# Kernel tuning notes

Measured on AMD Instinct MI355X. Metric: run time of the kernel, lower is better.

The kernel has to match this reference:

```python
import jax, jax.numpy as jnp
import numpy as np

EPS = 1e-3  # keras LayerNormalization default epsilon


def _ln(x, g, b):
    m = jnp.mean(x, axis=-1, keepdims=True)
    v = jnp.mean(jnp.square(x - m), axis=-1, keepdims=True)
    return (x - m) * jax.lax.rsqrt(v + EPS) * g + b


def setup_inputs() -> dict:
    key = jax.random.key(0)
    B, T, C, H = 64, 256, 1024, 16
    D = C // H
    ks = jax.random.split(key, 16)
    s = 0.02
    return {
        "x": jax.random.normal(ks[0], (B, T, C), jnp.float32),
        # per-head q/k/v projections (no bias), stacked over heads [H, C, D]
        "wq": jax.random.normal(ks[1], (H, C, D), jnp.float32) * s,
        "wk": jax.random.normal(ks[2], (H, C, D), jnp.float32) * s,
        "wv": jax.random.normal(ks[3], (H, C, D), jnp.float32) * s,
        "w_proj": jax.random.normal(ks[4], (C, C), jnp.float32) * s,
        "b_proj": jnp.zeros((C,), jnp.float32),
        # FFN: C -> 4C (relu) -> C
        "w1": jax.random.normal(ks[5], (C, 4 * C), jnp.float32) * s,
        "b1": jnp.zeros((4 * C,), jnp.float32),
        "w2": jax.random.normal(ks[6], (4 * C, C), jnp.float32) * s,
        "b2": jnp.zeros((C,), jnp.float32),
        # LayerNorm params: ln1 (pre-attn), ln2 (pre-ffn), ln3 (inside FeedForward)
        "g1": jnp.ones((C,), jnp.float32), "be1": jnp.zeros((C,), jnp.float32),
        "g2": jnp.ones((C,), jnp.float32), "be2": jnp.zeros((C,), jnp.float32),
        "g3": jnp.ones((C,), jnp.float32), "be3": jnp.zeros((C,), jnp.float32),
    }


def reference(x, wq, wk, wv, w_proj, b_proj, w1, b1, w2, b2,
              g1, be1, g2, be2, g3, be3):
    B, T, C = x.shape
    # --- multi-head causal self-attention on LN1(x) ---
    h = _ln(x, g1, be1)
    q = jnp.einsum('btc,hcd->bhtd', h, wq)
    k = jnp.einsum('btc,hcd->bhtd', h, wk)
    v = jnp.einsum('btc,hcd->bhtd', h, wv)
    # NOTE: original scales by C**-0.5 with C = n_embd (full dim), not head_size
    scores = jnp.einsum('bhtd,bhsd->bhts', q, k) * (C ** -0.5)
    causal = jnp.tril(jnp.ones((T, T), dtype=bool))
    scores = jnp.where(causal, scores, -jnp.inf)
    attn = jax.nn.softmax(scores, axis=-1)  # dropout is identity at inference
    out = jnp.einsum('bhts,bhsd->bhtd', attn, v)
    out = out.transpose(0, 2, 1, 3).reshape(B, T, C)  # concat heads
    out = out @ w_proj + b_proj
    x = x + out
    # --- FeedForward block (contains its own residual + LayerNorm) ---
    y = _ln(x, g2, be2)
    z = jax.nn.relu(y @ w1 + b1) @ w2 + b2
    return x + _ln(y + z, g3, be3)
```

## Files before the change

### kernel.cpp

```cpp
#include <hip/hip_runtime.h>

typedef __bf16 bf16_t;
typedef __bf16 bf16x8 __attribute__((ext_vector_type(8)));
typedef float f32x4 __attribute__((ext_vector_type(4)));

#define LN_EPS 1e-3f

__device__ __forceinline__ void gload_lds16(const void* g, void* l) {
    __builtin_amdgcn_global_load_lds(
        (__attribute__((address_space(1))) void*)(g),
        (__attribute__((address_space(3))) void*)(l), 16, 0, 0);
}

__global__ __launch_bounds__(256)
void transpose_f32_bf16(const float* __restrict__ in, bf16_t* __restrict__ outp,
                        int ldi, int ldo)
{
    __shared__ float tile[64][65];
    const int k0 = blockIdx.x * 64, n0 = blockIdx.y * 64;
    const int tid = threadIdx.x;
    const int r = tid >> 2;
    const int q = tid & 3;
    const float* src = in + (long)(k0 + r) * ldi + n0 + q * 16;
#pragma unroll
    for (int j = 0; j < 4; ++j) {
        float4 v = *(const float4*)(src + j * 4);
        tile[r][q * 16 + j * 4 + 0] = v.x;
        tile[r][q * 16 + j * 4 + 1] = v.y;
        tile[r][q * 16 + j * 4 + 2] = v.z;
        tile[r][q * 16 + j * 4 + 3] = v.w;
    }
    __syncthreads();
    union { bf16_t e[16]; uint4 u[2]; } pk;
#pragma unroll
    for (int j = 0; j < 16; ++j) pk.e[j] = (bf16_t)tile[q * 16 + j][r];
    bf16_t* dst = outp + (long)(n0 + r) * ldo + k0 + q * 16;
    *(uint4*)(dst)     = pk.u[0];
    *(uint4*)(dst + 8) = pk.u[1];
}

__global__ __launch_bounds__(256)
void pack_qkv_t(const float* __restrict__ wq, const float* __restrict__ wk,
                const float* __restrict__ wv, bf16_t* __restrict__ outp)
{
    __shared__ float tile[64][65];
    const int m   = blockIdx.y;
    const int sel = m >> 4, h = m & 15;
    const float* in = ((sel == 0) ? wq : (sel == 1) ? wk : wv) + (long)h * 65536;
    bf16_t* out = outp + ((long)sel * 1024 + h * 64) * 1024;
    const int k0 = blockIdx.x * 64;
    const int tid = threadIdx.x;
    const int r = tid >> 2;
    const int q = tid & 3;
    const float* src = in + (long)(k0 + r) * 64 + q * 16;
#pragma unroll
    for (int j = 0; j < 4; ++j) {
        float4 v = *(const float4*)(src + j * 4);
        tile[r][q * 16 + j * 4 + 0] = v.x;
        tile[r][q * 16 + j * 4 + 1] = v.y;
        tile[r][q * 16 + j * 4 + 2] = v.z;
        tile[r][q * 16 + j * 4 + 3] = v.w;
    }
    __syncthreads();
    union { bf16_t e[16]; uint4 u[2]; } pk;
#pragma unroll
    for (int j = 0; j < 16; ++j) pk.e[j] = (bf16_t)tile[q * 16 + j][r];
    bf16_t* dst = out + (long)r * 1024 + k0 + q * 16;
    *(uint4*)(dst)     = pk.u[0];
    *(uint4*)(dst + 8) = pk.u[1];
}

__global__ __launch_bounds__(256)
void ln_fwd(const float* __restrict__ in, const float* __restrict__ g,
            const float* __restrict__ be, bf16_t* __restrict__ outp)
{
    const long row = blockIdx.x;
    const int t = threadIdx.x;
    float4 v = ((const float4*)(in + row * 1024))[t];
    float s  = v.x + v.y + v.z + v.w;
    float sq = v.x * v.x + v.y * v.y + v.z * v.z + v.w * v.w;
#pragma unroll
    for (int off = 1; off < 64; off <<= 1) {
        s  += __shfl_xor(s, off);
        sq += __shfl_xor(sq, off);
    }
    __shared__ float red[8];
    if ((t & 63) == 0) { red[(t >> 6) * 2] = s; red[(t >> 6) * 2 + 1] = sq; }
    __syncthreads();
    s  = red[0] + red[2] + red[4] + red[6];
    sq = red[1] + red[3] + red[5] + red[7];
    float mean = s * 0.0009765625f;
    float var  = sq * 0.0009765625f - mean * mean;
    float rstd = rsqrtf(var + LN_EPS);
    float4 gv = ((const float4*)g)[t];
    float4 bv = ((const float4*)be)[t];
    union { bf16_t h[4]; uint2 u; } pk;
    pk.h[0] = (bf16_t)((v.x - mean) * rstd * gv.x + bv.x);
    pk.h[1] = (bf16_t)((v.y - mean) * rstd * gv.y + bv.y);
    pk.h[2] = (bf16_t)((v.z - mean) * rstd * gv.z + bv.z);
    pk.h[3] = (bf16_t)((v.w - mean) * rstd * gv.w + bv.w);
    *(uint2*)(outp + row * 1024 + t * 4) = pk.u;
}

__global__ __launch_bounds__(256)
void ln3_kernel(const bf16_t* __restrict__ in, const float* __restrict__ g,
                const float* __restrict__ be, float* outp, const float* res)
{
    const long row = blockIdx.x;
    const int t = threadIdx.x;
    union { uint2 u; bf16_t h[4]; } pk;
    pk.u = *(const uint2*)(in + row * 1024 + t * 4);
    float v0 = (float)pk.h[0], v1 = (float)pk.h[1], v2 = (float)pk.h[2], v3 = (float)pk.h[3];
    float s  = v0 + v1 + v2 + v3;
    float sq = v0 * v0 + v1 * v1 + v2 * v2 + v3 * v3;
#pragma unroll
    for (int off = 1; off < 64; off <<= 1) {
        s  += __shfl_xor(s, off);
        sq += __shfl_xor(sq, off);
    }
    __shared__ float red[8];
    if ((t & 63) == 0) { red[(t >> 6) * 2] = s; red[(t >> 6) * 2 + 1] = sq; }
    __syncthreads();
    s  = red[0] + red[2] + red[4] + red[6];
    sq = red[1] + red[3] + red[5] + red[7];
    float mean = s * 0.0009765625f;
    float var  = sq * 0.0009765625f - mean * mean;
    float rstd = rsqrtf(var + LN_EPS);
    float4 gv = ((const float4*)g)[t];
    float4 bv = ((const float4*)be)[t];
    float4 rv = ((const float4*)(res + row * 1024))[t];
    float4 ov;
    ov.x = rv.x + (v0 - mean) * rstd * gv.x + bv.x;
    ov.y = rv.y + (v1 - mean) * rstd * gv.y + bv.y;
    ov.z = rv.z + (v2 - mean) * rstd * gv.z + bv.z;
    ov.w = rv.w + (v3 - mean) * rstd * gv.w + bv.w;
    ((float4*)outp)[row * 256 + t] = ov;
}

template<int MODE>
__global__ __launch_bounds__(512, 2)
void gemm_bt(const bf16_t* __restrict__ Ap, const bf16_t* __restrict__ Bp,
             void* outp, const float* __restrict__ bias,
             const void* addp, int M, int N, int K)
{
    __shared__ __attribute__((aligned(16))) bf16_t As0[256 * 64];
    __shared__ __attribute__((aligned(16))) bf16_t As1[256 * 64];
    __shared__ __attribute__((aligned(16))) bf16_t As2[256 * 64];
    __shared__ __attribute__((aligned(16))) bf16_t Bs0[256 * 64];
    __shared__ __attribute__((aligned(16))) bf16_t Bs1[256 * 64];

    const int tid  = threadIdx.x;
    const int w    = tid >> 6, lane = tid & 63;
    const int l16  = lane & 15, lg = lane >> 4;
    const int wm   = w >> 2, wn = w & 3;
    const int srow = lane >> 3;
    const int sslot = lane & 7;

    const int gx  = gridDim.x;
    const int gy  = gridDim.y;
    const int nwg = gx * gy;
    const int bid = blockIdx.y * gx + blockIdx.x;
    const int cpx = nwg >> 3;
    const int sid = (bid & 7) * cpx + (bid >> 3);
    const long m0 = (long)(sid / gy) * 256;
    const long n0 = (long)(sid % gy) * 256;
    const int nkt = K >> 6;

    f32x4 acc[8][4] = {};
    bf16x8 a[4][2], b0[2][2], b1[2][2];

    auto STAGEH = [&](const bf16_t* src, long row0, int kt, bf16_t* dst, int h) {
#pragma unroll
        for (int i = 0; i < 2; ++i) {
            int r  = h * 128 + w * 16 + i * 8 + srow;
            int ss = sslot ^ (r & 7);
            gload_lds16(src + (row0 + r) * (long)K + (long)kt * 64 + ss * 8,
                        dst + (h * 128 + w * 16 + i * 8) * 64);
        }
    };

#define LDA_M(buf, mh) do {                                               \
    _Pragma("unroll") for (int j = 0; j < 4; ++j)                         \
    _Pragma("unroll") for (int kk = 0; kk < 2; ++kk) {                    \
        int r  = wm * 128 + (mh) * 64 + j * 16 + l16;                     \
        int ss = (kk * 4 + lg) ^ (r & 7);                                 \
        a[j][kk] = *(const bf16x8*)&buf[r * 64 + ss * 8];                 \
    } } while (0)

#define LDB_M(dst, buf, nh) do {                                          \
    _Pragma("unroll") for (int n = 0; n < 2; ++n)                         \
    _Pragma("unroll") for (int kk = 0; kk < 2; ++kk) {                    \
        int r  = wn * 64 + ((nh) * 2 + n) * 16 + l16;                     \
        int ss = (kk * 4 + lg) ^ (r & 7);                                 \
        dst[n][kk] = *(const bf16x8*)&buf[r * 64 + ss * 8];               \
    } } while (0)

#define MMA_M(bv, mh, nh) do {                                            \
    __builtin_amdgcn_s_setprio(1);                                        \
    _Pragma("unroll") for (int j = 0; j < 4; ++j)                         \
    _Pragma("unroll") for (int n = 0; n < 2; ++n)                         \
    _Pragma("unroll") for (int kk = 0; kk < 2; ++kk)                      \
        acc[(mh) * 4 + j][(nh) * 2 + n] =                                 \
            __builtin_amdgcn_mfma_f32_16x16x32_bf16(                      \
                a[j][kk], bv[n][kk], acc[(mh) * 4 + j][(nh) * 2 + n],     \
                0, 0, 0);                                                 \
    __builtin_amdgcn_s_setprio(0);                                        \
} while (0)

#define PRE_MFMA() do { __builtin_amdgcn_s_barrier();                     \
    asm volatile("s_waitcnt lgkmcnt(0)" ::: "memory");                    \
    __builtin_amdgcn_sched_barrier(0); } while (0)

    STAGEH(Ap, m0, 0, As0, 0); STAGEH(Ap, m0, 0, As0, 1);
    STAGEH(Bp, n0, 0, Bs0, 0); STAGEH(Bp, n0, 0, Bs0, 1);
    STAGEH(Ap, m0, 1, As1, 0); STAGEH(Ap, m0, 1, As1, 1);
    asm volatile("s_waitcnt vmcnt(0)" ::: "memory");
    __builtin_amdgcn_s_barrier();
    __builtin_amdgcn_sched_barrier(0);

    bf16_t *Ar = As0, *An1 = As1, *An2 = As2;
    bf16_t *Br = Bs0, *Bw = Bs1;

    for (int c = 0; c < nkt; ++c) {
        const bool pfa = (c + 2 < nkt);
        const bool pfb = (c + 1 < nkt);

        LDA_M(Ar, 0); LDB_M(b0, Br, 0);
        if (pfb) { STAGEH(Bp, n0, c + 1, Bw, 0); STAGEH(Bp, n0, c + 1, Bw, 1); }
        if (pfa) STAGEH(Ap, m0, c + 2, An2, 0);
        PRE_MFMA(); MMA_M(b0, 0, 0); __builtin_amdgcn_s_barrier();
        LDB_M(b1, Br, 1);
        PRE_MFMA(); MMA_M(b1, 0, 1); __builtin_amdgcn_s_barrier();
        LDA_M(Ar, 1);
        if (pfa) STAGEH(Ap, m0, c + 2, An2, 1);
        PRE_MFMA(); MMA_M(b1, 1, 1); __builtin_amdgcn_s_barrier();
        if (pfa) { asm volatile("s_waitcnt vmcnt(4)" ::: "memory"); }
        else     { asm volatile("s_waitcnt vmcnt(0)" ::: "memory"); }
        __builtin_amdgcn_s_barrier();
        __builtin_amdgcn_sched_barrier(0);
        MMA_M(b0, 1, 0); __builtin_amdgcn_s_barrier();

        bf16_t* t = Ar; Ar = An1; An1 = An2; An2 = t;
        t = Br; Br = Bw; Bw = t;
    }

#pragma unroll
    for (int fm = 0; fm < 8; ++fm) {
#pragma unroll
        for (int fn = 0; fn < 4; ++fn) {
            const long gcol = n0 + wn * 64 + fn * 16 + l16;
            float bv = 0.f;
            if (MODE != 0 && MODE != 4) bv = bias[gcol];
            const long grow0 = m0 + wm * 128 + fm * 16 + lg * 4;
            if (MODE == 4 && gcol >= 2048) {
                union { bf16_t h[4]; uint2 u; } pk;
#pragma unroll
                for (int e = 0; e < 4; ++e) pk.h[e] = (bf16_t)acc[fm][fn][e];
                const int hh = (int)(gcol >> 6) - 32;
                const int d  = (int)gcol & 63;
                const long bb = grow0 >> 8;
                const int s0  = (int)grow0 & 255;
                *(uint2*)((bf16_t*)addp + ((bb * 16 + hh) * 64 + d) * 256 + s0) = pk.u;
                continue;
            }
#pragma unroll
            for (int e = 0; e < 4; ++e) {
                const long grow = grow0 + e;
                float v = acc[fm][fn][e];
                if (MODE == 0 || MODE == 4) {
                    ((bf16_t*)outp)[grow * N + gcol] = (bf16_t)v;
                } else if (MODE == 1) {
                    v += bv + ((const float*)addp)[grow * N + gcol];
                    ((float*)outp)[grow * N + gcol] = v;
                } else if (MODE == 2) {
                    v += bv; v = v > 0.f ? v : 0.f;
                    ((bf16_t*)outp)[grow * N + gcol] = (bf16_t)v;
                } else {
                    v += bv + (float)((const bf16_t*)addp)[grow * N + gcol];
                    ((bf16_t*)outp)[grow * N + gcol] = (bf16_t)v;
                }
            }
        }
    }
#undef LDA_M
#undef LDB_M
#undef MMA_M
#undef PRE_MFMA
}

__global__ __launch_bounds__(256)
void attn_kernel(const bf16_t* __restrict__ qkv, const bf16_t* __restrict__ vt,
                 bf16_t* __restrict__ outp)
{
    __shared__ __attribute__((aligned(16))) bf16_t Kt[2][64 * 64];
    __shared__ __attribute__((aligned(16))) bf16_t Vt[2][64 * 64];
    __shared__ __attribute__((aligned(16))) bf16_t Ps[4][16 * 72];

    const int tid = threadIdx.x, w = tid >> 6, lane = tid & 63;
    const int l16 = lane & 15, lg = lane >> 4;
    const int b = blockIdx.x >> 4, hh = blockIdx.x & 15;
    const bf16_t* pq = qkv + (long)(b * 256) * 3072 + hh * 64;
    const bf16_t* pv = vt + (long)blockIdx.x * 64 * 256;
    const int sr8 = lane >> 3;
    const int sl  = lane & 7;

    bf16x8 qf[4][2];
#pragma unroll
    for (int fm = 0; fm < 4; ++fm)
#pragma unroll
        for (int kk = 0; kk < 2; ++kk)
            qf[fm][kk] = *(const bf16x8*)(pq + (long)(fm * 64 + w * 16 + l16) * 3072
                                          + kk * 32 + lg * 8);

    f32x4 o[4][4] = {};
    float mrun[4][4], lrun[4][4];
#pragma unroll
    for (int i = 0; i < 4; ++i)
#pragma unroll
        for (int j = 0; j < 4; ++j) { mrun[i][j] = -__builtin_inff(); lrun[i][j] = 0.f; }

    auto STAGE = [&](int st, int bb) {
#pragma unroll
        for (int i = 0; i < 2; ++i) {
            int r  = w * 16 + i * 8 + sr8;
            int ss = sl ^ (r & 7);
            gload_lds16(pq + (long)(st * 64 + r) * 3072 + 1024 + ss * 8,
                        &Kt[bb][(w * 16 + i * 8) * 64]);
            gload_lds16(pv + (long)r * 256 + st * 64 + ss * 8,
                        &Vt[bb][(w * 16 + i * 8) * 64]);
        }
    };

    STAGE(0, 0);
    asm volatile("s_waitcnt vmcnt(0)" ::: "memory");
    __syncthreads();

#pragma unroll
    for (int st = 0; st < 4; ++st) {
        const int cb = st & 1;
        if (st < 3) STAGE(st + 1, cb ^ 1);

        f32x4 s[4][4] = {};
#pragma unroll
        for (int ks = 0; ks < 2; ++ks) {
            bf16x8 kb[4];
#pragma unroll
            for (int fs = 0; fs < 4; ++fs)
                kb[fs] = *(const bf16x8*)&Kt[cb][(fs * 16 + l16) * 64
                                               + ((ks * 4 + lg) ^ (l16 & 7)) * 8];
#pragma unroll
            for (int fm = 0; fm < 4; ++fm) {
                if (fm < st) continue;
#pragma unroll
                for (int fs = 0; fs < 4; ++fs)
                    s[fm][fs] = __builtin_amdgcn_mfma_f32_16x16x32_bf16(
                        qf[fm][ks], kb[fs], s[fm][fs], 0, 0, 0);
            }
        }

#pragma unroll
        for (int fm = 0; fm < 4; ++fm) {
            if (fm < st) continue;
#pragma unroll
            for (int fs = 0; fs < 4; ++fs)
#pragma unroll
                for (int e = 0; e < 4; ++e) {
                    float v = s[fm][fs][e] * 0.03125f;
                    if (st == fm && (fs * 16 + l16) > (w * 16 + lg * 4 + e))
                        v = -__builtin_inff();
                    s[fm][fs][e] = v;
                }
#pragma unroll
            for (int e = 0; e < 4; ++e) {
                float pm = fmaxf(fmaxf(s[fm][0][e], s[fm][1][e]),
                                 fmaxf(s[fm][2][e], s[fm][3][e]));
#pragma unroll
                for (int off = 1; off < 16; off <<= 1) pm = fmaxf(pm, __shfl_xor(pm, off));
                float mnew  = fmaxf(mrun[fm][e], pm);
                float alpha = __expf(mrun[fm][e] - mnew);
                float rs = 0.f;
#pragma unroll
                for (int fs = 0; fs < 4; ++fs) {
                    float p = __expf(s[fm][fs][e] - mnew);
                    s[fm][fs][e] = p;
                    rs += p;
                }
#pragma unroll
                for (int off = 1; off < 16; off <<= 1) rs += __shfl_xor(rs, off);
                lrun[fm][e] = lrun[fm][e] * alpha + rs;
                mrun[fm][e] = mnew;
#pragma unroll
                for (int fd = 0; fd < 4; ++fd) o[fm][fd][e] *= alpha;
            }
#pragma unroll
            for (int fs = 0; fs < 4; ++fs)
#pragma unroll
                for (int e = 0; e < 4; ++e)
                    Ps[w][(lg * 4 + e) * 72 + fs * 16 + l16] = (bf16_t)s[fm][fs][e];
            bf16x8 ap0 = *(const bf16x8*)&Ps[w][l16 * 72 + lg * 8];
            bf16x8 ap1 = *(const bf16x8*)&Ps[w][l16 * 72 + 32 + lg * 8];
#pragma unroll
            for (int fd = 0; fd < 4; ++fd) {
                bf16x8 vb0 = *(const bf16x8*)&Vt[cb][(fd * 16 + l16) * 64
                                                    + ((lg) ^ (l16 & 7)) * 8];
                bf16x8 vb1 = *(const bf16x8*)&Vt[cb][(fd * 16 + l16) * 64
                                                    + ((4 + lg) ^ (l16 & 7)) * 8];
                o[fm][fd] = __builtin_amdgcn_mfma_f32_16x16x32_bf16(ap0, vb0, o[fm][fd], 0, 0, 0);
                o[fm][fd] = __builtin_amdgcn_mfma_f32_16x16x32_bf16(ap1, vb1, o[fm][fd], 0, 0, 0);
            }
        }
        asm volatile("s_waitcnt vmcnt(0)" ::: "memory");
        __syncthreads();
    }

#pragma unroll
    for (int fm = 0; fm < 4; ++fm)
#pragma unroll
        for (int e = 0; e < 4; ++e) {
            float inv = 1.f / lrun[fm][e];
            long row = (long)b * 256 + fm * 64 + w * 16 + lg * 4 + e;
#pragma unroll
            for (int fd = 0; fd < 4; ++fd)
                outp[row * 1024 + hh * 64 + fd * 16 + l16] =
                    (bf16_t)(o[fm][fd][e] * inv);
        }
}

extern "C" void kernel_launch(void* const* d_in, const int* in_sizes, int n_in,
                              void* d_out, int out_size, void* d_ws, size_t ws_size,
                              hipStream_t stream)
{
    (void)in_sizes; (void)n_in; (void)out_size; (void)ws_size;
    const float* x      = (const float*)d_in[0];
    const float* wq     = (const float*)d_in[1];
    const float* wk     = (const float*)d_in[2];
    const float* wv     = (const float*)d_in[3];
    const float* w_proj = (const float*)d_in[4];
    const float* b_proj = (const float*)d_in[5];
    const float* w1     = (const float*)d_in[6];
    const float* b1     = (const float*)d_in[7];
    const float* w2     = (const float*)d_in[8];
    const float* b2     = (const float*)d_in[9];
    const float* g1  = (const float*)d_in[10]; const float* be1 = (const float*)d_in[11];
    const float* g2  = (const float*)d_in[12]; const float* be2 = (const float*)d_in[13];
    const float* g3  = (const float*)d_in[14]; const float* be3 = (const float*)d_in[15];

    char* ws = (char*)d_ws;
    bf16_t* wqkv  = (bf16_t*)(ws + 0);
    bf16_t* wproj = (bf16_t*)(ws + 6291456);
    bf16_t* w1t   = (bf16_t*)(ws + 8388608);
    bf16_t* w2t   = (bf16_t*)(ws + 16777216);
    bf16_t* h     = (bf16_t*)(ws + 25165824);
    bf16_t* qkv   = (bf16_t*)(ws + 58720256);
    bf16_t* attn  = h;
    bf16_t* u     = h;
    bf16_t* y     = (bf16_t*)(ws + 159383552);
    bf16_t* vt    = y;
    float*  x2    = (float*)d_out;
    bf16_t* tbuf  = y;

    const int M = 16384;

    transpose_f32_bf16<<<dim3(16, 16), 256, 0, stream>>>(w_proj, wproj, 1024, 1024);
    transpose_f32_bf16<<<dim3(16, 64), 256, 0, stream>>>(w1, w1t, 4096, 1024);
    transpose_f32_bf16<<<dim3(64, 16), 256, 0, stream>>>(w2, w2t, 1024, 4096);
    pack_qkv_t<<<dim3(16, 48), 256, 0, stream>>>(wq, wk, wv, wqkv);

    ln_fwd<<<M, 256, 0, stream>>>(x, g1, be1, h);
    gemm_bt<4><<<dim3(64, 12), 512, 0, stream>>>(h, wqkv, qkv, nullptr, vt, M, 3072, 1024);
    attn_kernel<<<1024, 256, 0, stream>>>(qkv, vt, attn);
    gemm_bt<1><<<dim3(64, 4), 512, 0, stream>>>(attn, wproj, x2, b_proj, x, M, 1024, 1024);
    ln_fwd<<<M, 256, 0, stream>>>(x2, g2, be2, y);
    gemm_bt<2><<<dim3(64, 16), 512, 0, stream>>>(y, w1t, u, b1, nullptr, M, 4096, 1024);
    gemm_bt<3><<<dim3(64, 4), 512, 0, stream>>>(u, w2t, tbuf, b2, y, M, 1024, 4096);
    ln3_kernel<<<M, 256, 0, stream>>>(tbuf, g3, be3, (float*)d_out, x2);
}
```

Before: 634.6 us.

## Deepen GEMM B prefetch to two tiles and preload all K/V in attention

In the GEMM main loop, B tiles are now prefetched two iterations ahead like A, written into the buffer just consumed, with the vmcnt wait raised to match. The attention kernel loads all four K/V stages into LDS up front, doubling its K/V buffers, and drops the per-stage waits and block syncs. This aims to hide global load latency and remove barriers, but it raises LDS use in attention (fewer resident blocks) and reuses the B read buffer while other waves may still be reading it.

```diff
diff --git a/kernel.cpp b/kernel.cpp
--- a/kernel.cpp
+++ b/kernel.cpp
@@ -213,7 +213,10 @@
 
     STAGEH(Ap, m0, 0, As0, 0); STAGEH(Ap, m0, 0, As0, 1);
     STAGEH(Bp, n0, 0, Bs0, 0); STAGEH(Bp, n0, 0, Bs0, 1);
-    STAGEH(Ap, m0, 1, As1, 0); STAGEH(Ap, m0, 1, As1, 1);
+    if (nkt > 1) {
+        STAGEH(Ap, m0, 1, As1, 0); STAGEH(Ap, m0, 1, As1, 1);
+        STAGEH(Bp, n0, 1, Bs1, 0); STAGEH(Bp, n0, 1, Bs1, 1);
+    }
     asm volatile("s_waitcnt vmcnt(0)" ::: "memory");
     __builtin_amdgcn_s_barrier();
     __builtin_amdgcn_sched_barrier(0);
@@ -222,20 +225,21 @@
     bf16_t *Br = Bs0, *Bw = Bs1;
 
     for (int c = 0; c < nkt; ++c) {
-        const bool pfa = (c + 2 < nkt);
-        const bool pfb = (c + 1 < nkt);
+        const bool pf = (c + 2 < nkt);
 
         LDA_M(Ar, 0); LDB_M(b0, Br, 0);
-        if (pfb) { STAGEH(Bp, n0, c + 1, Bw, 0); STAGEH(Bp, n0, c + 1, Bw, 1); }
-        if (pfa) STAGEH(Ap, m0, c + 2, An2, 0);
+        if (pf) STAGEH(Ap, m0, c + 2, An2, 0);
         PRE_MFMA(); MMA_M(b0, 0, 0); __builtin_amdgcn_s_barrier();
         LDB_M(b1, Br, 1);
         PRE_MFMA(); MMA_M(b1, 0, 1); __builtin_amdgcn_s_barrier();
         LDA_M(Ar, 1);
-        if (pfa) STAGEH(Ap, m0, c + 2, An2, 1);
+        if (pf) {
+            STAGEH(Ap, m0, c + 2, An2, 1);
+            STAGEH(Bp, n0, c + 2, Br, 0); STAGEH(Bp, n0, c + 2, Br, 1);
+        }
         PRE_MFMA(); MMA_M(b1, 1, 1); __builtin_amdgcn_s_barrier();
-        if (pfa) { asm volatile("s_waitcnt vmcnt(4)" ::: "memory"); }
-        else     { asm volatile("s_waitcnt vmcnt(0)" ::: "memory"); }
+        if (pf) { asm volatile("s_waitcnt vmcnt(8)" ::: "memory"); }
+        else    { asm volatile("s_waitcnt vmcnt(0)" ::: "memory"); }
         __builtin_amdgcn_s_barrier();
         __builtin_amdgcn_sched_barrier(0);
         MMA_M(b0, 1, 0); __builtin_amdgcn_s_barrier();
@@ -292,8 +296,8 @@
 void attn_kernel(const bf16_t* __restrict__ qkv, const bf16_t* __restrict__ vt,
                  bf16_t* __restrict__ outp)
 {
-    __shared__ __attribute__((aligned(16))) bf16_t Kt[2][64 * 64];
-    __shared__ __attribute__((aligned(16))) bf16_t Vt[2][64 * 64];
+    __shared__ __attribute__((aligned(16))) bf16_t Kt[4][64 * 64];
+    __shared__ __attribute__((aligned(16))) bf16_t Vt[4][64 * 64];
     __shared__ __attribute__((aligned(16))) bf16_t Ps[4][16 * 72];
 
     const int tid = threadIdx.x, w = tid >> 6, lane = tid & 63;
@@ -312,42 +316,37 @@
             qf[fm][kk] = *(const bf16x8*)(pq + (long)(fm * 64 + w * 16 + l16) * 3072
                                           + kk * 32 + lg * 8);
 
-    f32x4 o[4][4] = {};
-    float mrun[4][4], lrun[4][4];
-#pragma unroll
-    for (int i = 0; i < 4; ++i)
-#pragma unroll
-        for (int j = 0; j < 4; ++j) { mrun[i][j] = -__builtin_inff(); lrun[i][j] = 0.f; }
-
-    auto STAGE = [&](int st, int bb) {
+#pragma unroll
+    for (int st = 0; st < 4; ++st)
 #pragma unroll
         for (int i = 0; i < 2; ++i) {
             int r  = w * 16 + i * 8 + sr8;
             int ss = sl ^ (r & 7);
             gload_lds16(pq + (long)(st * 64 + r) * 3072 + 1024 + ss * 8,
-                        &Kt[bb][(w * 16 + i * 8) * 64]);
+                        &Kt[st][(w * 16 + i * 8) * 64]);
             gload_lds16(pv + (long)r * 256 + st * 64 + ss * 8,
-                        &Vt[bb][(w * 16 + i * 8) * 64]);
-        }
-    };
-
-    STAGE(0, 0);
+                        &Vt[st][(w * 16 + i * 8) * 64]);
+        }
     asm volatile("s_waitcnt vmcnt(0)" ::: "memory");
     __syncthreads();
 
+    f32x4 o[4][4] = {};
+    float mrun[4][4], lrun[4][4];
+#pragma unroll
+    for (int i = 0; i < 4; ++i)
+#pragma unroll
+        for (int j = 0; j < 4; ++j) { mrun[i][j] = -__builtin_inff(); lrun[i][j] = 0.f; }
+
 #pragma unroll
     for (int st = 0; st < 4; ++st) {
-        const int cb = st & 1;
-        if (st < 3) STAGE(st + 1, cb ^ 1);
-
         f32x4 s[4][4] = {};
 #pragma unroll
         for (int ks = 0; ks < 2; ++ks) {
             bf16x8 kb[4];
 #pragma unroll
             for (int fs = 0; fs < 4; ++fs)
-                kb[fs] = *(const bf16x8*)&Kt[cb][(fs * 16 + l16) * 64
-                                               + ((ks * 4 + lg) ^ (l16 & 7)) * 8];
+                kb[fs] = *(const bf16x8*)&Kt[st][(fs * 16 + l16) * 64
+                                                + ((ks * 4 + lg) ^ (l16 & 7)) * 8];
 #pragma unroll
             for (int fm = 0; fm < 4; ++fm) {
                 if (fm < st) continue;
@@ -401,16 +400,14 @@
             bf16x8 ap1 = *(const bf16x8*)&Ps[w][l16 * 72 + 32 + lg * 8];
 #pragma unroll
             for (int fd = 0; fd < 4; ++fd) {
-                bf16x8 vb0 = *(const bf16x8*)&Vt[cb][(fd * 16 + l16) * 64
+                bf16x8 vb0 = *(const bf16x8*)&Vt[st][(fd * 16 + l16) * 64
                                                     + ((lg) ^ (l16 & 7)) * 8];
-                bf16x8 vb1 = *(const bf16x8*)&Vt[cb][(fd * 16 + l16) * 64
+                bf16x8 vb1 = *(const bf16x8*)&Vt[st][(fd * 16 + l16) * 64
                                                     + ((4 + lg) ^ (l16 & 7)) * 8];
                 o[fm][fd] = __builtin_amdgcn_mfma_f32_16x16x32_bf16(ap0, vb0, o[fm][fd], 0, 0, 0);
                 o[fm][fd] = __builtin_amdgcn_mfma_f32_16x16x32_bf16(ap1, vb1, o[fm][fd], 0, 0, 0);
             }
         }
-        asm volatile("s_waitcnt vmcnt(0)" ::: "memory");
-        __syncthreads();
     }
 
 #pragma unroll
```

After: 647.7 us. 1.02x slower.
